# Kernel tuning notes

Hardware: AMD Instinct MI355X
Metric: run time of the kernel (lower is better)

Reference implementation:

```python
import jax, jax.numpy as jnp
import numpy as np

PATCH_LEN = 16
PATCH_STRIDE = 8
DIM = 512
NUM_HEADS = 8
HEAD_DIM = DIM // NUM_HEADS
NUM_LAYERS = 4
MLP_HIDDEN = 4 * DIM
ROPE_BASE = 10000.0
LN_EPS = 1e-5


def setup_inputs() -> dict:
    key = jax.random.key(0)
    ks = jax.random.split(key, 20)
    B, T, C = 4, 8192, 7
    s = 0.02
    inp = {
        "x": jax.random.normal(ks[0], (B, T, C), dtype=jnp.float32),
        "W_emb": jax.random.normal(ks[1], (PATCH_LEN * C, DIM), dtype=jnp.float32) * s,
        "b_emb": jnp.zeros((DIM,), jnp.float32),
        "ln1_g": jnp.ones((NUM_LAYERS, DIM), jnp.float32),
        "ln1_b": jnp.zeros((NUM_LAYERS, DIM), jnp.float32),
        "W_qkv": jax.random.normal(ks[2], (NUM_LAYERS, DIM, 3 * DIM), dtype=jnp.float32) * s,
        "b_qkv": jnp.zeros((NUM_LAYERS, 3 * DIM), jnp.float32),
        "W_proj": jax.random.normal(ks[3], (NUM_LAYERS, DIM, DIM), dtype=jnp.float32) * s,
        "b_proj": jnp.zeros((NUM_LAYERS, DIM), jnp.float32),
        "ln2_g": jnp.ones((NUM_LAYERS, DIM), jnp.float32),
        "ln2_b": jnp.zeros((NUM_LAYERS, DIM), jnp.float32),
        "W_mlp1": jax.random.normal(ks[4], (NUM_LAYERS, DIM, MLP_HIDDEN), dtype=jnp.float32) * s,
        "b_mlp1": jnp.zeros((NUM_LAYERS, MLP_HIDDEN), jnp.float32),
        "W_mlp2": jax.random.normal(ks[5], (NUM_LAYERS, MLP_HIDDEN, DIM), dtype=jnp.float32) * s,
        "b_mlp2": jnp.zeros((NUM_LAYERS, DIM), jnp.float32),
        "lnf_g": jnp.ones((DIM,), jnp.float32),
        "lnf_b": jnp.zeros((DIM,), jnp.float32),
    }
    return inp


def _layer_norm(x, g, b):
    mu = jnp.mean(x, axis=-1, keepdims=True)
    var = jnp.mean(jnp.square(x - mu), axis=-1, keepdims=True)
    return (x - mu) * jax.lax.rsqrt(var + LN_EPS) * g + b


def _rotate_half(x):
    x1, x2 = jnp.split(x, 2, axis=-1)
    return jnp.concatenate((-x2, x1), axis=-1)


def _rope_cos_sin(seq_len):
    t = jnp.arange(seq_len, dtype=jnp.float32)
    inv_freq = 1.0 / (ROPE_BASE ** (jnp.arange(0, HEAD_DIM, 2, dtype=jnp.float32) / HEAD_DIM))
    freqs = jnp.outer(t, inv_freq)                      # [L, hd/2]
    emb = jnp.concatenate((freqs, freqs), axis=-1)      # [L, hd]
    return jnp.cos(emb), jnp.sin(emb)


def _forward(x, W_emb, b_emb, ln1_g, ln1_b, W_qkv, b_qkv, W_proj, b_proj,
             ln2_g, ln2_b, W_mlp1, b_mlp1, W_mlp2, b_mlp2, lnf_g, lnf_b):
    B, T, C = x.shape
    n = (T - PATCH_LEN) // PATCH_STRIDE + 1
    # torch unfold: [B, n, C, patch_len], then flattened as (C, patch_len)
    idx = jnp.arange(n)[:, None] * PATCH_STRIDE + jnp.arange(PATCH_LEN)[None, :]  # [n, P]
    patches = x[:, idx, :]                              # [B, n, P, C]
    patches = patches.transpose(0, 1, 3, 2).reshape(B, n, C * PATCH_LEN)
    emb = patches @ W_emb + b_emb                       # [B, n, D]

    cos, sin = _rope_cos_sin(n)                         # [n, hd]
    cos = cos[None, None, :, :]
    sin = sin[None, None, :, :]
    scale = HEAD_DIM ** -0.5

    h = emb
    for i in range(NUM_LAYERS):
        # --- attention ---
        y = _layer_norm(h, ln1_g[i], ln1_b[i])
        qkv = (y @ W_qkv[i] + b_qkv[i]).reshape(B, n, 3, NUM_HEADS, HEAD_DIM)
        qkv = qkv.transpose(2, 0, 3, 1, 4)              # [3, B, H, n, hd]
        q, k, v = qkv[0], qkv[1], qkv[2]
        q = q * cos + _rotate_half(q) * sin
        k = k * cos + _rotate_half(k) * sin
        attn = jax.nn.softmax(jnp.einsum('bhqd,bhkd->bhqk', q, k) * scale, axis=-1)
        o = jnp.einsum('bhqk,bhkd->bhqd', attn, v)      # [B, H, n, hd]
        o = o.transpose(0, 2, 1, 3).reshape(B, n, DIM)
        h = h + (o @ W_proj[i] + b_proj[i])
        # --- mlp ---
        y = _layer_norm(h, ln2_g[i], ln2_b[i])
        y = jax.nn.gelu(y @ W_mlp1[i] + b_mlp1[i], approximate=False)
        h = h + (y @ W_mlp2[i] + b_mlp2[i])

    x_out = _layer_norm(h, lnf_g, lnf_b)
    return emb, x_out


def reference(x, W_emb, b_emb, ln1_g, ln1_b, W_qkv, b_qkv, W_proj, b_proj,
              ln2_g, ln2_b, W_mlp1, b_mlp1, W_mlp2, b_mlp2, lnf_g, lnf_b):
    return _forward(x, W_emb, b_emb, ln1_g, ln1_b, W_qkv, b_qkv, W_proj, b_proj,
                    ln2_g, ln2_b, W_mlp1, b_mlp1, W_mlp2, b_mlp2, lnf_g, lnf_b)
```

## Files before the change

kernel.cpp:

```cpp
#include <hip/hip_runtime.h>
#include <hip/hip_bf16.h>
#include <math.h>

#define B_SZ 4
#define T_LEN 8192
#define C_IN 7
#define NPATCH 1023
#define DIM 512
#define NH 8
#define HD 64
#define NLAYERS 4
#define MLP_HID 2048
#define M_ROWS (B_SZ * NPATCH)
#define KEMB 128
#define LN_EPS 1e-5f

typedef __attribute__((ext_vector_type(8))) short short8;
typedef __attribute__((ext_vector_type(4))) float float4v;

static __device__ __forceinline__ unsigned short f2bf(float f) {
  __hip_bfloat16 h = __float2bfloat16(f);
  return *reinterpret_cast<unsigned short*>(&h);
}
static __device__ __forceinline__ float bf2f(unsigned short u) {
  return __uint_as_float(((unsigned)u) << 16);
}

static __device__ __forceinline__ void gload_lds16(const void* g, void* l) {
  __builtin_amdgcn_global_load_lds(
      (const __attribute__((address_space(1))) unsigned int*)g,
      (__attribute__((address_space(3))) unsigned int*)l, 16, 0, 0);
}

__global__ __launch_bounds__(256) void patch_kernel(
    const float* __restrict__ x, unsigned short* __restrict__ Pm) {
  int idx = blockIdx.x * 256 + threadIdx.x;
  if (idx >= M_ROWS * KEMB) return;
  int row = idx >> 7, c = idx & 127;
  float v = 0.f;
  if (c < 112) {
    int b = row / NPATCH, i = row - b * NPATCH;
    int ci = c >> 4, p = c & 15;
    v = x[((size_t)b * T_LEN + (size_t)i * 8 + p) * C_IN + ci];
  }
  Pm[idx] = f2bf(v);
}

__global__ __launch_bounds__(256) void wemb_cvt_kernel(
    const float* __restrict__ W, unsigned short* __restrict__ Wt) {
  int idx = blockIdx.x * 256 + threadIdx.x;
  if (idx >= DIM * KEMB) return;
  int n = idx >> 7, k = idx & 127;
  float v = (k < 112) ? W[(size_t)k * DIM + n] : 0.f;
  Wt[idx] = f2bf(v);
}

template <bool BF>
__global__ __launch_bounds__(256) void ln_kernel(
    const float* __restrict__ in, const float* __restrict__ g,
    const float* __restrict__ bb, void* __restrict__ outv, int M) {
  int row = blockIdx.x * 4 + (threadIdx.x >> 6);
  if (row >= M) return;
  int lane = threadIdx.x & 63;
  const float* xr = in + (size_t)row * DIM;
  float v[8];
  float s = 0.f;
  #pragma unroll
  for (int k = 0; k < 8; ++k) { v[k] = xr[lane + 64 * k]; s += v[k]; }
  #pragma unroll
  for (int off = 32; off; off >>= 1) s += __shfl_down(s, off);
  s = __shfl(s, 0);
  float mu = s * (1.f / DIM);
  float q = 0.f;
  #pragma unroll
  for (int k = 0; k < 8; ++k) { float d = v[k] - mu; q = fmaf(d, d, q); }
  #pragma unroll
  for (int off = 32; off; off >>= 1) q += __shfl_down(q, off);
  q = __shfl(q, 0);
  float rstd = rsqrtf(q * (1.f / DIM) + LN_EPS);
  #pragma unroll
  for (int k = 0; k < 8; ++k) {
    int d = lane + 64 * k;
    float r = (v[k] - mu) * rstd * g[d] + bb[d];
    if (BF)
      ((unsigned short*)outv)[(size_t)row * DIM + d] = f2bf(r);
    else
      ((float*)outv)[(size_t)row * DIM + d] = r;
  }
}

__global__ __launch_bounds__(256) void wcvt_kernel(
    const float* __restrict__ W, unsigned short* __restrict__ Wt, int K, int N) {
  __shared__ float tile[32][33];
  int n0 = blockIdx.x * 32, k0 = blockIdx.y * 32, L = blockIdx.z;
  const float* Ws = W + (size_t)L * K * N;
  unsigned short* Wd = Wt + (size_t)L * K * N;
  int tx = threadIdx.x & 31, ty = threadIdx.x >> 5;
  #pragma unroll
  for (int i = 0; i < 4; ++i)
    tile[ty + i * 8][tx] = Ws[(size_t)(k0 + ty + i * 8) * N + n0 + tx];
  __syncthreads();
  #pragma unroll
  for (int i = 0; i < 4; ++i)
    Wd[(size_t)(n0 + ty + i * 8) * K + k0 + tx] = f2bf(tile[tx][ty + i * 8]);
}

__global__ __launch_bounds__(256) void rope_tab_kernel(float2* __restrict__ tab) {
  int idx = blockIdx.x * 256 + threadIdx.x;
  if (idx >= NPATCH * 32) return;
  int i = idx >> 5, j = idx & 31;
  float inv = powf(10000.0f, -(float)j * (1.0f / 32.0f));
  float sn, cs;
  sincosf((float)i * inv, &sn, &cs);
  tab[idx] = make_float2(cs, sn);
}

template <int TM, int TN, int EPI>
__global__ __launch_bounds__(256) void mfma_gemm(
    const unsigned short* __restrict__ A, const unsigned short* __restrict__ Bt,
    const float* __restrict__ bias, const float* __restrict__ res,
    float* __restrict__ Cf, float* __restrict__ Cf2,
    unsigned short* __restrict__ Cb, const float2* __restrict__ rtab,
    int M, int N, int K) {
  constexpr int WM = TM / 2, WN = TN / 2;
  constexpr int NI = WM / 16, NJ = WN / 16;
  constexpr int NCH = (TM + TN) / 16;
  constexpr int CPW = NCH / 4;
  __shared__ __align__(16) unsigned short As[2][TM][32];
  __shared__ __align__(16) unsigned short Bs[2][TN][32];
  const int bm = blockIdx.y * TM;
  const int bn = blockIdx.x * TN;
  const int tid = threadIdx.x;
  const int lane = tid & 63, wave = tid >> 6;
  const int quad = lane >> 4, l16 = lane & 15;
  const int wm = (wave & 1) * WM;
  const int wn = (wave >> 1) * WN;
  const int lrow4 = lane >> 2, lc = lane & 3;
  const int rslot = quad ^ ((l16 >> 1) & 3);

  float4v acc[NI][NJ];
  #pragma unroll
  for (int i = 0; i < NI; ++i)
    #pragma unroll
    for (int j = 0; j < NJ; ++j)
      acc[i][j] = (float4v){0.f, 0.f, 0.f, 0.f};

  auto stage = [&](int bufI, int kk) {
    #pragma unroll
    for (int it = 0; it < CPW; ++it) {
      int c = wave * CPW + it;
      if (c < TM / 16) {
        int row = c * 16 + lrow4;
        int col16 = lc ^ ((row >> 1) & 3);
        gload_lds16(A + (size_t)(bm + row) * K + kk + col16 * 8,
                    &As[bufI][c * 16][0]);
      } else {
        int c2 = c - TM / 16;
        int row = c2 * 16 + lrow4;
        int col16 = lc ^ ((row >> 1) & 3);
        gload_lds16(Bt + (size_t)(bn + row) * K + kk + col16 * 8,
                    &Bs[bufI][c2 * 16][0]);
      }
    }
  };

  stage(0, 0);
  int buf = 0;
  for (int k0 = 0; k0 < K; k0 += 32, buf ^= 1) {
    __syncthreads();
    if (k0 + 32 < K) stage(buf ^ 1, k0 + 32);
    short8 af[NI], bfr[NJ];
    #pragma unroll
    for (int i = 0; i < NI; ++i)
      af[i] = *(const short8*)&As[buf][wm + i * 16 + l16][rslot * 8];
    #pragma unroll
    for (int j = 0; j < NJ; ++j)
      bfr[j] = *(const short8*)&Bs[buf][wn + j * 16 + l16][rslot * 8];
    __builtin_amdgcn_s_setprio(1);
    #pragma unroll
    for (int i = 0; i < NI; ++i)
      #pragma unroll
      for (int j = 0; j < NJ; ++j)
        acc[i][j] = __builtin_amdgcn_mfma_f32_16x16x32_bf16(
            af[i], bfr[j], acc[i][j], 0, 0, 0);
    __builtin_amdgcn_s_setprio(0);
  }

  if (EPI == 6) {
    const int sec = (bn + wn) >> 9;
    #pragma unroll
    for (int i = 0; i < NI; ++i) {
      int gm0 = bm + wm + i * 16 + quad * 4;
      #pragma unroll
      for (int r = 0; r < 4; ++r) {
        int gm = gm0 + r;
        if (gm >= M) continue;
        size_t rowoff = (size_t)gm * N;
        if (sec < 2) {
          int ip = gm; if (ip >= 2046) ip -= 2046; if (ip >= 1023) ip -= 1023;
          float sc = (sec == 0) ? 0.125f : 1.f;
          #pragma unroll
          for (int j = 0; j < NJ / 2; ++j) {
            int gn = bn + wn + j * 16 + l16;
            float v0 = acc[i][j][r] + bias[gn];
            float v1 = acc[i][j + NJ / 2][r] + bias[gn + 32];
            float2 t = rtab[ip * 32 + j * 16 + l16];
            Cb[rowoff + gn]      = f2bf((v0 * t.x - v1 * t.y) * sc);
            Cb[rowoff + gn + 32] = f2bf((v1 * t.x + v0 * t.y) * sc);
          }
        } else {
          #pragma unroll
          for (int j = 0; j < NJ; ++j) {
            int gn = bn + wn + j * 16 + l16;
            Cb[rowoff + gn] = f2bf(acc[i][j][r] + bias[gn]);
          }
        }
      }
    }
    return;
  }

  #pragma unroll
  for (int j = 0; j < NJ; ++j) {
    int gn = bn + wn + j * 16 + l16;
    float bv = bias[gn];
    #pragma unroll
    for (int i = 0; i < NI; ++i) {
      int gm0 = bm + wm + i * 16 + quad * 4;
      #pragma unroll
      for (int r = 0; r < 4; ++r) {
        int gm = gm0 + r;
        if (gm < M) {
          float v = acc[i][j][r] + bv;
          size_t off = (size_t)gm * N + gn;
          if (EPI == 1) {
            Cf[off] = v + res[off];
          } else if (EPI == 2) {
            Cb[off] = f2bf(0.5f * v * (1.f + erff(v * 0.70710678118f)));
          } else if (EPI == 3) {
            Cb[off] = f2bf(v);
          } else {
            Cf[off] = v;
            Cf2[off] = v;
          }
        }
      }
    }
  }
}

#define APITCH 72

__global__ __launch_bounds__(512, 4) void attn_kernel(
    const unsigned short* __restrict__ qkvb, unsigned short* __restrict__ o) {
  const int bid = blockIdx.x;
  const int xcd = bid & 7, slot = bid >> 3;
  const int qt0 = (slot & 15) * 64;
  const int gh = xcd + 8 * (slot >> 4);
  const int h = gh & 7, b = gh >> 3;

  const int tid = threadIdx.x;
  const int lane = tid & 63, wave = tid >> 6;
  const int quad = lane >> 4, l16 = lane & 15;
  const int half = wave >> 2, wq = wave & 3;

  __shared__ __align__(16) unsigned short Ks[2][64][APITCH];
  __shared__ __align__(16) unsigned short Vt[2][64][APITCH];
  __shared__ __align__(16) unsigned short Ps[8][16][APITCH];

  short8 aq0 = {0, 0, 0, 0, 0, 0, 0, 0}, aq1 = aq0;
  {
    int qrow = qt0 + wq * 16 + l16;
    if (qrow < NPATCH) {
      const uint4* qr = (const uint4*)(qkvb + (size_t)(b * NPATCH + qrow) * (3 * DIM) + h * HD + quad * 8);
      aq0 = __builtin_bit_cast(short8, qr[0]);
      aq1 = __builtin_bit_cast(short8, qr[4]);
    }
  }

  const int krow = tid >> 2, kc0 = (tid & 3) * 16;
  const int kp2 = tid & 63, dg = tid >> 6;
  uint4 pk0, pk1, pv0, pv1;
  auto load_kv = [&](int js) {
    pk0 = pk1 = pv0 = pv1 = make_uint4(0u, 0u, 0u, 0u);
    int jk = js + krow;
    if (jk < NPATCH) {
      const unsigned short* kb = qkvb + (size_t)(b * NPATCH + jk) * (3 * DIM) + DIM + h * HD;
      pk0 = *(const uint4*)(kb + kc0);
      pk1 = *(const uint4*)(kb + kc0 + 8);
    }
    int jv = js + 2 * kp2;
    const unsigned short* vb = qkvb + (size_t)(b * NPATCH + jv) * (3 * DIM) + 2 * DIM + h * HD + dg * 8;
    if (jv < NPATCH)     pv0 = *(const uint4*)vb;
    if (jv + 1 < NPATCH) pv1 = *(const uint4*)(vb + 3 * DIM);
  };

  load_kv(0);

  float4v accO[4];
  #pragma unroll
  for (int j2 = 0; j2 < 4; ++j2) accO[j2] = (float4v){0.f, 0.f, 0.f, 0.f};
  float m_run[4] = {-1e30f, -1e30f, -1e30f, -1e30f};
  float lp[4] = {0.f, 0.f, 0.f, 0.f};

  constexpr int NIT = (NPATCH + 127) / 128;
  for (int it = 0; it < NIT; ++it) {
    if (it > 0) __syncthreads();
    {
      *(uint4*)&Ks[krow >> 6][krow & 63][kc0] = pk0;
      *(uint4*)&Ks[krow >> 6][krow & 63][kc0 + 8] = pk1;
      unsigned short va[8], vb8[8];
      *(uint4*)&va[0] = pv0;
      *(uint4*)&vb8[0] = pv1;
      const int vh = kp2 >> 5, lp2 = kp2 & 31;
      #pragma unroll
      for (int u = 0; u < 8; ++u) {
        unsigned pk = (unsigned)va[u] | ((unsigned)vb8[u] << 16);
        *(unsigned*)&Vt[vh][dg * 8 + u][2 * lp2] = pk;
      }
    }
    __syncthreads();
    if (it + 1 < NIT) load_kv((it + 1) * 128);

    const int j0 = it * 128 + half * 64;

    float4v s[4];
    __builtin_amdgcn_s_setprio(1);
    #pragma unroll
    for (int j = 0; j < 4; ++j) {
      s[j] = (float4v){0.f, 0.f, 0.f, 0.f};
      short8 bk0 = *(const short8*)&Ks[half][j * 16 + l16][quad * 8];
      short8 bk1 = *(const short8*)&Ks[half][j * 16 + l16][32 + quad * 8];
      s[j] = __builtin_amdgcn_mfma_f32_16x16x32_bf16(aq0, bk0, s[j], 0, 0, 0);
      s[j] = __builtin_amdgcn_mfma_f32_16x16x32_bf16(aq1, bk1, s[j], 0, 0, 0);
    }
    __builtin_amdgcn_s_setprio(0);

    float mx[4];
    #pragma unroll
    for (int r = 0; r < 4; ++r)
      mx[r] = fmaxf(fmaxf(s[0][r], s[1][r]), fmaxf(s[2][r], s[3][r]));
    #pragma unroll
    for (int mask = 1; mask < 16; mask <<= 1)
      #pragma unroll
      for (int r = 0; r < 4; ++r)
        mx[r] = fmaxf(mx[r], __shfl_xor(mx[r], mask));
    float gmax = fmaxf(fmaxf(mx[0] - m_run[0], mx[1] - m_run[1]),
                       fmaxf(mx[2] - m_run[2], mx[3] - m_run[3]));
    if (!__all(gmax <= 8.f)) {
      #pragma unroll
      for (int r = 0; r < 4; ++r) {
        float mnew = fmaxf(m_run[r], mx[r]);
        float al = __expf(m_run[r] - mnew);
        m_run[r] = mnew;
        lp[r] *= al;
        #pragma unroll
        for (int j2 = 0; j2 < 4; ++j2) accO[j2][r] *= al;
      }
    }
    #pragma unroll
    for (int j = 0; j < 4; ++j) {
      bool valid = (j0 + j * 16 + l16) < NPATCH;
      #pragma unroll
      for (int r = 0; r < 4; ++r) {
        float p = valid ? __expf(s[j][r] - m_run[r]) : 0.f;
        lp[r] += p;
        Ps[wave][quad * 4 + r][j * 16 + l16] = f2bf(p);
      }
    }

    short8 pa0 = *(const short8*)&Ps[wave][l16][quad * 8];
    short8 pa1 = *(const short8*)&Ps[wave][l16][32 + quad * 8];
    __builtin_amdgcn_s_setprio(1);
    #pragma unroll
    for (int j2 = 0; j2 < 4; ++j2) {
      short8 v0 = *(const short8*)&Vt[half][j2 * 16 + l16][quad * 8];
      short8 v1 = *(const short8*)&Vt[half][j2 * 16 + l16][32 + quad * 8];
      accO[j2] = __builtin_amdgcn_mfma_f32_16x16x32_bf16(pa0, v0, accO[j2], 0, 0, 0);
      accO[j2] = __builtin_amdgcn_mfma_f32_16x16x32_bf16(pa1, v1, accO[j2], 0, 0, 0);
    }
    __builtin_amdgcn_s_setprio(0);
  }

  #pragma unroll
  for (int mask = 1; mask < 16; mask <<= 1)
    #pragma unroll
    for (int r = 0; r < 4; ++r)
      lp[r] += __shfl_xor(lp[r], mask);

  float* Pf = (float*)&Ps[0][0][0];
  __syncthreads();
  if (half == 1) {
    #pragma unroll
    for (int j2 = 0; j2 < 4; ++j2)
      #pragma unroll
      for (int r = 0; r < 4; ++r)
        Pf[((wq * 64 + lane) << 4) + j2 * 4 + r] = accO[j2][r];
    if (l16 == 0) {
      #pragma unroll
      for (int r = 0; r < 4; ++r) {
        Pf[4096 + ((wq * 16 + quad * 4 + r) << 1)]     = m_run[r];
        Pf[4096 + ((wq * 16 + quad * 4 + r) << 1) + 1] = lp[r];
      }
    }
  }
  __syncthreads();
  if (half == 0) {
    #pragma unroll
    for (int r = 0; r < 4; ++r) {
      float m1 = Pf[4096 + ((wq * 16 + quad * 4 + r) << 1)];
      float l1 = Pf[4096 + ((wq * 16 + quad * 4 + r) << 1) + 1];
      float M = fmaxf(m_run[r], m1);
      float w0 = __expf(m_run[r] - M), w1 = __expf(m1 - M);
      float inv = 1.f / (w0 * lp[r] + w1 * l1);
      int qi = qt0 + wq * 16 + quad * 4 + r;
      if (qi < NPATCH) {
        size_t off = (size_t)(b * NPATCH + qi) * DIM + h * HD + l16;
        #pragma unroll
        for (int j2 = 0; j2 < 4; ++j2) {
          float a1 = Pf[((wq * 64 + lane) << 4) + j2 * 4 + r];
          o[off + j2 * 16] = f2bf((w0 * accO[j2][r] + w1 * a1) * inv);
        }
      }
    }
  }
}

extern "C" void kernel_launch(void* const* d_in, const int* in_sizes, int n_in,
                              void* d_out, int out_size, void* d_ws, size_t ws_size,
                              hipStream_t stream) {
  const float* x      = (const float*)d_in[0];
  const float* W_emb  = (const float*)d_in[1];
  const float* b_emb  = (const float*)d_in[2];
  const float* ln1_g  = (const float*)d_in[3];
  const float* ln1_b  = (const float*)d_in[4];
  const float* W_qkv  = (const float*)d_in[5];
  const float* b_qkv  = (const float*)d_in[6];
  const float* W_proj = (const float*)d_in[7];
  const float* b_proj = (const float*)d_in[8];
  const float* ln2_g  = (const float*)d_in[9];
  const float* ln2_b  = (const float*)d_in[10];
  const float* W_mlp1 = (const float*)d_in[11];
  const float* b_mlp1 = (const float*)d_in[12];
  const float* W_mlp2 = (const float*)d_in[13];
  const float* b_mlp2 = (const float*)d_in[14];
  const float* lnf_g  = (const float*)d_in[15];
  const float* lnf_b  = (const float*)d_in[16];
  float* out = (float*)d_out;

  float* h              = (float*)d_ws;
  unsigned short* qkvb  = (unsigned short*)(h + (size_t)M_ROWS * DIM);
  unsigned short* midbf = qkvb;
  unsigned short* ybf   = qkvb + (size_t)M_ROWS * MLP_HID;
  unsigned short* obf   = ybf;
  unsigned short* wqkv_t  = ybf + (size_t)M_ROWS * DIM;
  unsigned short* wproj_t = wqkv_t  + (size_t)NLAYERS * DIM * 3 * DIM;
  unsigned short* wmlp1_t = wproj_t + (size_t)NLAYERS * DIM * DIM;
  unsigned short* wmlp2_t = wmlp1_t + (size_t)NLAYERS * DIM * MLP_HID;
  float2* rtab = (float2*)(wmlp2_t + (size_t)NLAYERS * MLP_HID * DIM);
  unsigned short* Pm    = (unsigned short*)(rtab + (size_t)NPATCH * 32);
  unsigned short* Wembt = Pm + (size_t)M_ROWS * KEMB;

  wcvt_kernel<<<dim3(3 * DIM / 32, DIM / 32, NLAYERS), 256, 0, stream>>>(W_qkv,  wqkv_t,  DIM, 3 * DIM);
  wcvt_kernel<<<dim3(DIM / 32, DIM / 32, NLAYERS),     256, 0, stream>>>(W_proj, wproj_t, DIM, DIM);
  wcvt_kernel<<<dim3(MLP_HID / 32, DIM / 32, NLAYERS), 256, 0, stream>>>(W_mlp1, wmlp1_t, DIM, MLP_HID);
  wcvt_kernel<<<dim3(DIM / 32, MLP_HID / 32, NLAYERS), 256, 0, stream>>>(W_mlp2, wmlp2_t, MLP_HID, DIM);
  rope_tab_kernel<<<(NPATCH * 32 + 255) / 256, 256, 0, stream>>>(rtab);
  patch_kernel<<<(M_ROWS * KEMB + 255) / 256, 256, 0, stream>>>(x, Pm);
  wemb_cvt_kernel<<<(DIM * KEMB + 255) / 256, 256, 0, stream>>>(W_emb, Wembt);

  const int MT64 = (M_ROWS + 63) / 64;
  const int MT128 = (M_ROWS + 127) / 128;
  const int LNG = (M_ROWS + 3) / 4;

  mfma_gemm<64, 64, 5><<<dim3(DIM / 64, MT64), 256, 0, stream>>>(
      Pm, Wembt, b_emb, nullptr, out, h, nullptr, nullptr, M_ROWS, DIM, KEMB);

  for (int L = 0; L < NLAYERS; ++L) {
    ln_kernel<true><<<LNG, 256, 0, stream>>>(h, ln1_g + L * DIM, ln1_b + L * DIM, ybf, M_ROWS);
    mfma_gemm<128, 128, 6><<<dim3(3 * DIM / 128, MT128), 256, 0, stream>>>(
        ybf, wqkv_t + (size_t)L * DIM * 3 * DIM, b_qkv + L * 3 * DIM,
        nullptr, nullptr, nullptr, qkvb, rtab, M_ROWS, 3 * DIM, DIM);
    attn_kernel<<<dim3(512), 512, 0, stream>>>(qkvb, obf);
    mfma_gemm<64, 64, 1><<<dim3(DIM / 64, MT64), 256, 0, stream>>>(
        obf, wproj_t + (size_t)L * DIM * DIM, b_proj + L * DIM,
        h, h, nullptr, nullptr, nullptr, M_ROWS, DIM, DIM);
    ln_kernel<true><<<LNG, 256, 0, stream>>>(h, ln2_g + L * DIM, ln2_b + L * DIM, ybf, M_ROWS);
    mfma_gemm<128, 128, 2><<<dim3(MLP_HID / 128, MT128), 256, 0, stream>>>(
        ybf, wmlp1_t + (size_t)L * DIM * MLP_HID, b_mlp1 + L * MLP_HID,
        nullptr, nullptr, nullptr, midbf, nullptr, M_ROWS, MLP_HID, DIM);
    mfma_gemm<64, 64, 1><<<dim3(DIM / 64, MT64), 256, 0, stream>>>(
        midbf, wmlp2_t + (size_t)L * MLP_HID * DIM, b_mlp2 + L * DIM,
        h, h, nullptr, nullptr, nullptr, M_ROWS, DIM, MLP_HID);
  }

  ln_kernel<false><<<LNG, 256, 0, stream>>>(h, lnf_g, lnf_b, out + (size_t)M_ROWS * DIM, M_ROWS);
}
```

Measured before the change: 644.2 us.

## Merge preprocessing kernels and add configurable K-step to GEMM tiles

Folds the seven weight-conversion, patching and RoPE-table launches into one block-partitioned prep kernel to cut launch overhead. The MFMA GEMM gains a KSTEP template parameter that sets how much K is staged per LDS buffer, with generalized swizzling. The N=512 GEMMs now use KSTEP 64 to halve barrier count per K, and the QKV GEMM switches to 64x128 tiles for more blocks. Doubling LDS per block may lower occupancy, and the reworked swizzle could introduce bank conflicts.

```diff
diff --git a/kernel.cpp b/kernel.cpp
--- a/kernel.cpp
+++ b/kernel.cpp
@@ -22,9 +22,6 @@
   __hip_bfloat16 h = __float2bfloat16(f);
   return *reinterpret_cast<unsigned short*>(&h);
 }
-static __device__ __forceinline__ float bf2f(unsigned short u) {
-  return __uint_as_float(((unsigned)u) << 16);
-}
 
 static __device__ __forceinline__ void gload_lds16(const void* g, void* l) {
   __builtin_amdgcn_global_load_lds(
@@ -32,27 +29,78 @@
       (__attribute__((address_space(3))) unsigned int*)l, 16, 0, 0);
 }
 
-__global__ __launch_bounds__(256) void patch_kernel(
-    const float* __restrict__ x, unsigned short* __restrict__ Pm) {
-  int idx = blockIdx.x * 256 + threadIdx.x;
-  if (idx >= M_ROWS * KEMB) return;
-  int row = idx >> 7, c = idx & 127;
-  float v = 0.f;
-  if (c < 112) {
-    int b = row / NPATCH, i = row - b * NPATCH;
-    int ci = c >> 4, p = c & 15;
-    v = x[((size_t)b * T_LEN + (size_t)i * 8 + p) * C_IN + ci];
-  }
-  Pm[idx] = f2bf(v);
-}
-
-__global__ __launch_bounds__(256) void wemb_cvt_kernel(
-    const float* __restrict__ W, unsigned short* __restrict__ Wt) {
-  int idx = blockIdx.x * 256 + threadIdx.x;
-  if (idx >= DIM * KEMB) return;
-  int n = idx >> 7, k = idx & 127;
-  float v = (k < 112) ? W[(size_t)k * DIM + n] : 0.f;
-  Wt[idx] = f2bf(v);
+#define PB0 3072
+#define PB1 4096
+#define PB2 8192
+#define PB3 12288
+#define PB4 14334
+#define PB5 14590
+#define PB6 14718
+
+__global__ __launch_bounds__(256) void prep_kernel(
+    const float* __restrict__ W_qkv, unsigned short* __restrict__ wqkv_t,
+    const float* __restrict__ W_proj, unsigned short* __restrict__ wproj_t,
+    const float* __restrict__ W_mlp1, unsigned short* __restrict__ wmlp1_t,
+    const float* __restrict__ W_mlp2, unsigned short* __restrict__ wmlp2_t,
+    const float* __restrict__ x, unsigned short* __restrict__ Pm,
+    const float* __restrict__ W_emb, unsigned short* __restrict__ Wembt,
+    float2* __restrict__ rtab) {
+  __shared__ float tile[32][33];
+  const int bid = blockIdx.x, tid = threadIdx.x;
+
+  auto do_wcvt = [&](const float* W, unsigned short* Wt, int K, int N,
+                     int t, int nx, int ny) {
+    int xb = t % nx, yb = (t / nx) % ny, L = t / (nx * ny);
+    int n0 = xb * 32, k0 = yb * 32;
+    const float* Ws = W + (size_t)L * K * N;
+    unsigned short* Wd = Wt + (size_t)L * K * N;
+    int tx = tid & 31, ty = tid >> 5;
+    #pragma unroll
+    for (int i = 0; i < 4; ++i)
+      tile[ty + i * 8][tx] = Ws[(size_t)(k0 + ty + i * 8) * N + n0 + tx];
+    __syncthreads();
+    #pragma unroll
+    for (int i = 0; i < 4; ++i)
+      Wd[(size_t)(n0 + ty + i * 8) * K + k0 + tx] = f2bf(tile[tx][ty + i * 8]);
+  };
+
+  if (bid < PB0) {
+    do_wcvt(W_qkv, wqkv_t, DIM, 3 * DIM, bid, 48, 16);
+  } else if (bid < PB1) {
+    do_wcvt(W_proj, wproj_t, DIM, DIM, bid - PB0, 16, 16);
+  } else if (bid < PB2) {
+    do_wcvt(W_mlp1, wmlp1_t, DIM, MLP_HID, bid - PB1, 64, 16);
+  } else if (bid < PB3) {
+    do_wcvt(W_mlp2, wmlp2_t, MLP_HID, DIM, bid - PB2, 16, 64);
+  } else if (bid < PB4) {
+    int idx = (bid - PB3) * 256 + tid;
+    if (idx < M_ROWS * KEMB) {
+      int row = idx >> 7, c = idx & 127;
+      float v = 0.f;
+      if (c < 112) {
+        int b = row / NPATCH, i = row - b * NPATCH;
+        int ci = c >> 4, p = c & 15;
+        v = x[((size_t)b * T_LEN + (size_t)i * 8 + p) * C_IN + ci];
+      }
+      Pm[idx] = f2bf(v);
+    }
+  } else if (bid < PB5) {
+    int idx = (bid - PB4) * 256 + tid;
+    if (idx < DIM * KEMB) {
+      int n = idx >> 7, k = idx & 127;
+      float v = (k < 112) ? W_emb[(size_t)k * DIM + n] : 0.f;
+      Wembt[idx] = f2bf(v);
+    }
+  } else {
+    int idx = (bid - PB5) * 256 + tid;
+    if (idx < NPATCH * 32) {
+      int i = idx >> 5, j = idx & 31;
+      float inv = powf(10000.0f, -(float)j * (1.0f / 32.0f));
+      float sn, cs;
+      sincosf((float)i * inv, &sn, &cs);
+      rtab[idx] = make_float2(cs, sn);
+    }
+  }
 }
 
 template <bool BF>
@@ -89,33 +137,7 @@
   }
 }
 
-__global__ __launch_bounds__(256) void wcvt_kernel(
-    const float* __restrict__ W, unsigned short* __restrict__ Wt, int K, int N) {
-  __shared__ float tile[32][33];
-  int n0 = blockIdx.x * 32, k0 = blockIdx.y * 32, L = blockIdx.z;
-  const float* Ws = W + (size_t)L * K * N;
-  unsigned short* Wd = Wt + (size_t)L * K * N;
-  int tx = threadIdx.x & 31, ty = threadIdx.x >> 5;
-  #pragma unroll
-  for (int i = 0; i < 4; ++i)
-    tile[ty + i * 8][tx] = Ws[(size_t)(k0 + ty + i * 8) * N + n0 + tx];
-  __syncthreads();
-  #pragma unroll
-  for (int i = 0; i < 4; ++i)
-    Wd[(size_t)(n0 + ty + i * 8) * K + k0 + tx] = f2bf(tile[tx][ty + i * 8]);
-}
-
-__global__ __launch_bounds__(256) void rope_tab_kernel(float2* __restrict__ tab) {
-  int idx = blockIdx.x * 256 + threadIdx.x;
-  if (idx >= NPATCH * 32) return;
-  int i = idx >> 5, j = idx & 31;
-  float inv = powf(10000.0f, -(float)j * (1.0f / 32.0f));
-  float sn, cs;
-  sincosf((float)i * inv, &sn, &cs);
-  tab[idx] = make_float2(cs, sn);
-}
-
-template <int TM, int TN, int EPI>
+template <int TM, int TN, int KSTEP, int EPI>
 __global__ __launch_bounds__(256) void mfma_gemm(
     const unsigned short* __restrict__ A, const unsigned short* __restrict__ Bt,
     const float* __restrict__ bias, const float* __restrict__ res,
@@ -124,10 +146,14 @@
     int M, int N, int K) {
   constexpr int WM = TM / 2, WN = TN / 2;
   constexpr int NI = WM / 16, NJ = WN / 16;
-  constexpr int NCH = (TM + TN) / 16;
-  constexpr int CPW = NCH / 4;
-  __shared__ __align__(16) unsigned short As[2][TM][32];
-  __shared__ __align__(16) unsigned short Bs[2][TN][32];
+  constexpr int RCH = KSTEP / 8;
+  constexpr int RPU = 64 / RCH;
+  constexpr int AU = TM / RPU;
+  constexpr int NU = (TM + TN) / RPU;
+  constexpr int CPW = NU / 4;
+  constexpr int SH = (KSTEP == 32) ? 1 : 0;
+  __shared__ __align__(16) unsigned short As[2][TM][KSTEP];
+  __shared__ __align__(16) unsigned short Bs[2][TN][KSTEP];
   const int bm = blockIdx.y * TM;
   const int bn = blockIdx.x * TN;
   const int tid = threadIdx.x;
@@ -135,8 +161,8 @@
   const int quad = lane >> 4, l16 = lane & 15;
   const int wm = (wave & 1) * WM;
   const int wn = (wave >> 1) * WN;
-  const int lrow4 = lane >> 2, lc = lane & 3;
-  const int rslot = quad ^ ((l16 >> 1) & 3);
+  const int lrow = lane / RCH, lc = lane & (RCH - 1);
+  const int rsw = (l16 >> SH) & (RCH - 1);
 
   float4v acc[NI][NJ];
   #pragma unroll
@@ -148,42 +174,48 @@
   auto stage = [&](int bufI, int kk) {
     #pragma unroll
     for (int it = 0; it < CPW; ++it) {
-      int c = wave * CPW + it;
-      if (c < TM / 16) {
-        int row = c * 16 + lrow4;
-        int col16 = lc ^ ((row >> 1) & 3);
+      int u = wave * CPW + it;
+      if (u < AU) {
+        int row = u * RPU + lrow;
+        int col16 = lc ^ ((row >> SH) & (RCH - 1));
         gload_lds16(A + (size_t)(bm + row) * K + kk + col16 * 8,
-                    &As[bufI][c * 16][0]);
+                    &As[bufI][u * RPU][0]);
       } else {
-        int c2 = c - TM / 16;
-        int row = c2 * 16 + lrow4;
-        int col16 = lc ^ ((row >> 1) & 3);
+        int row = (u - AU) * RPU + lrow;
+        int col16 = lc ^ ((row >> SH) & (RCH - 1));
         gload_lds16(Bt + (size_t)(bn + row) * K + kk + col16 * 8,
-                    &Bs[bufI][c2 * 16][0]);
+                    &Bs[bufI][(u - AU) * RPU][0]);
       }
     }
   };
 
   stage(0, 0);
   int buf = 0;
-  for (int k0 = 0; k0 < K; k0 += 32, buf ^= 1) {
+  for (int k0 = 0; k0 < K; k0 += KSTEP, buf ^= 1) {
     __syncthreads();
-    if (k0 + 32 < K) stage(buf ^ 1, k0 + 32);
-    short8 af[NI], bfr[NJ];
-    #pragma unroll
-    for (int i = 0; i < NI; ++i)
-      af[i] = *(const short8*)&As[buf][wm + i * 16 + l16][rslot * 8];
-    #pragma unroll
-    for (int j = 0; j < NJ; ++j)
-      bfr[j] = *(const short8*)&Bs[buf][wn + j * 16 + l16][rslot * 8];
-    __builtin_amdgcn_s_setprio(1);
-    #pragma unroll
-    for (int i = 0; i < NI; ++i)
-      #pragma unroll
-      for (int j = 0; j < NJ; ++j)
-        acc[i][j] = __builtin_amdgcn_mfma_f32_16x16x32_bf16(
-            af[i], bfr[j], acc[i][j], 0, 0, 0);
-    __builtin_amdgcn_s_setprio(0);
+    if (k0 + KSTEP < K) stage(buf ^ 1, k0 + KSTEP);
+    #pragma unroll
+    for (int t = 0; t < KSTEP / 32; ++t) {
+      short8 af[NI], bfr[NJ];
+      #pragma unroll
+      for (int i = 0; i < NI; ++i) {
+        int rslot = (t * 4 + quad) ^ rsw;
+        af[i] = *(const short8*)&As[buf][wm + i * 16 + l16][rslot * 8];
+      }
+      #pragma unroll
+      for (int j = 0; j < NJ; ++j) {
+        int rslot = (t * 4 + quad) ^ rsw;
+        bfr[j] = *(const short8*)&Bs[buf][wn + j * 16 + l16][rslot * 8];
+      }
+      __builtin_amdgcn_s_setprio(1);
+      #pragma unroll
+      for (int i = 0; i < NI; ++i)
+        #pragma unroll
+        for (int j = 0; j < NJ; ++j)
+          acc[i][j] = __builtin_amdgcn_mfma_f32_16x16x32_bf16(
+              af[i], bfr[j], acc[i][j], 0, 0, 0);
+      __builtin_amdgcn_s_setprio(0);
+    }
   }
 
   if (EPI == 6) {
@@ -461,35 +493,31 @@
   unsigned short* Pm    = (unsigned short*)(rtab + (size_t)NPATCH * 32);
   unsigned short* Wembt = Pm + (size_t)M_ROWS * KEMB;
 
-  wcvt_kernel<<<dim3(3 * DIM / 32, DIM / 32, NLAYERS), 256, 0, stream>>>(W_qkv,  wqkv_t,  DIM, 3 * DIM);
-  wcvt_kernel<<<dim3(DIM / 32, DIM / 32, NLAYERS),     256, 0, stream>>>(W_proj, wproj_t, DIM, DIM);
-  wcvt_kernel<<<dim3(MLP_HID / 32, DIM / 32, NLAYERS), 256, 0, stream>>>(W_mlp1, wmlp1_t, DIM, MLP_HID);
-  wcvt_kernel<<<dim3(DIM / 32, MLP_HID / 32, NLAYERS), 256, 0, stream>>>(W_mlp2, wmlp2_t, MLP_HID, DIM);
-  rope_tab_kernel<<<(NPATCH * 32 + 255) / 256, 256, 0, stream>>>(rtab);
-  patch_kernel<<<(M_ROWS * KEMB + 255) / 256, 256, 0, stream>>>(x, Pm);
-  wemb_cvt_kernel<<<(DIM * KEMB + 255) / 256, 256, 0, stream>>>(W_emb, Wembt);
+  prep_kernel<<<dim3(PB6), 256, 0, stream>>>(
+      W_qkv, wqkv_t, W_proj, wproj_t, W_mlp1, wmlp1_t, W_mlp2, wmlp2_t,
+      x, Pm, W_emb, Wembt, rtab);
 
   const int MT64 = (M_ROWS + 63) / 64;
   const int MT128 = (M_ROWS + 127) / 128;
   const int LNG = (M_ROWS + 3) / 4;
 
-  mfma_gemm<64, 64, 5><<<dim3(DIM / 64, MT64), 256, 0, stream>>>(
+  mfma_gemm<64, 64, 64, 5><<<dim3(DIM / 64, MT64), 256, 0, stream>>>(
       Pm, Wembt, b_emb, nullptr, out, h, nullptr, nullptr, M_ROWS, DIM, KEMB);
 
   for (int L = 0; L < NLAYERS; ++L) {
     ln_kernel<true><<<LNG, 256, 0, stream>>>(h, ln1_g + L * DIM, ln1_b + L * DIM, ybf, M_ROWS);
-    mfma_gemm<128, 128, 6><<<dim3(3 * DIM / 128, MT128), 256, 0, stream>>>(
+    mfma_gemm<64, 128, 32, 6><<<dim3(3 * DIM / 128, MT64), 256, 0, stream>>>(
         ybf, wqkv_t + (size_t)L * DIM * 3 * DIM, b_qkv + L * 3 * DIM,
         nullptr, nullptr, nullptr, qkvb, rtab, M_ROWS, 3 * DIM, DIM);
     attn_kernel<<<dim3(512), 512, 0, stream>>>(qkvb, obf);
-    mfma_gemm<64, 64, 1><<<dim3(DIM / 64, MT64), 256, 0, stream>>>(
+    mfma_gemm<64, 64, 64, 1><<<dim3(DIM / 64, MT64), 256, 0, stream>>>(
         obf, wproj_t + (size_t)L * DIM * DIM, b_proj + L * DIM,
         h, h, nullptr, nullptr, nullptr, M_ROWS, DIM, DIM);
     ln_kernel<true><<<LNG, 256, 0, stream>>>(h, ln2_g + L * DIM, ln2_b + L * DIM, ybf, M_ROWS);
-    mfma_gemm<128, 128, 2><<<dim3(MLP_HID / 128, MT128), 256, 0, stream>>>(
+    mfma_gemm<128, 128, 32, 2><<<dim3(MLP_HID / 128, MT128), 256, 0, stream>>>(
         ybf, wmlp1_t + (size_t)L * DIM * MLP_HID, b_mlp1 + L * MLP_HID,
         nullptr, nullptr, nullptr, midbf, nullptr, M_ROWS, MLP_HID, DIM);
-    mfma_gemm<64, 64, 1><<<dim3(DIM / 64, MT64), 256, 0, stream>>>(
+    mfma_gemm<64, 64, 64, 1><<<dim3(DIM / 64, MT64), 256, 0, stream>>>(
         midbf, wmlp2_t + (size_t)L * MLP_HID * DIM, b_mlp2 + L * DIM,
         h, h, nullptr, nullptr, nullptr, M_ROWS, DIM, MLP_HID);
   }
```

Result: faster. 612.3 us (-4.9%).
